# Performance work log

Hardware: AMD Instinct MI355X
Metric: run time of the kernel (lower is better)

The kernel has to match this reference:

```python
import jax, jax.numpy as jnp
import numpy as np

ALPHA = 0.2          # leaky_relu negative slope
NEG_INF = -9e15      # mask fill value (matches torch source)


def setup_inputs() -> dict:
    key = jax.random.key(0)
    k_h, k_mask, k_W, k_a = jax.random.split(key, 4)
    B, N, F_in, F_out = 4, 65536, 128, 128
    h = jax.random.normal(k_h, (B, N, F_in), dtype=jnp.float32)
    # op_mask > 0 means "mask out this neighbor" (prev/self/next)
    op_mask = jax.random.randint(k_mask, (B, N, 3), 0, 2, dtype=jnp.int32)
    # xavier_uniform-style init for params
    lim_W = 1.414 * np.sqrt(6.0 / (F_in + F_out))
    W = jax.random.uniform(k_W, (F_in, F_out), dtype=jnp.float32, minval=-lim_W, maxval=lim_W)
    lim_a = 1.414 * np.sqrt(6.0 / (2 * F_out + 1))
    a = jax.random.uniform(k_a, (2 * F_out, 1), dtype=jnp.float32, minval=-lim_a, maxval=lim_a)
    return {"h": h, "op_mask": op_mask, "W": W, "a": a}


def reference(h, op_mask, W, a):
    F_out = W.shape[1]
    Wh = jnp.matmul(h, W)                                   # [B, N, F]
    # windowed neighbors: prev (roll +1), self, next (roll -1)
    Wh_concat = jnp.stack(
        [jnp.roll(Wh, 1, axis=1), Wh, jnp.roll(Wh, -1, axis=1)], axis=-2
    )                                                       # [B, N, 3, F]
    Wh1 = jnp.matmul(Wh, a[:F_out])                         # [B, N, 1]
    Wh2 = jnp.matmul(Wh, a[F_out:])                         # [B, N, 1]
    Wh2_concat = jnp.stack(
        [jnp.roll(Wh2, 1, axis=1), Wh2, jnp.roll(Wh2, -1, axis=1)], axis=-1
    )                                                       # [B, N, 1, 3]
    e = jax.nn.leaky_relu(Wh1[..., None] + Wh2_concat, ALPHA)  # [B, N, 1, 3]
    e = jnp.where(op_mask[:, :, None, :] > 0, jnp.float32(NEG_INF), e)
    attention = jax.nn.softmax(e, axis=-1)                  # [B, N, 1, 3]
    # dropout_prob = 0.0 (eval-equivalent), so dropout is identity
    h_new = jnp.matmul(attention, Wh_concat).squeeze(-2)    # [B, N, F]
    return h_new
```

## Files before the change

### kernel.cpp

```cpp
#include <hip/hip_runtime.h>
#include <hip/hip_bf16.h>

typedef __attribute__((ext_vector_type(8))) short short8;
typedef __attribute__((ext_vector_type(4))) float f32x4;

#define ALPHA 0.2f
#define NEG_INF -9e15f
#define OUT_ROWS 126

__device__ __forceinline__ unsigned short f2bf(float x) {
    union { float f; unsigned int u; } v; v.f = x;
    unsigned int r = v.u + 0x7FFFu + ((v.u >> 16) & 1u);
    return (unsigned short)(r >> 16);
}

__global__ __launch_bounds__(256, 2)
void gat_fused(const float* __restrict__ h, const int* __restrict__ opm,
               const float* __restrict__ W, const float* __restrict__ a,
               float* __restrict__ out, int N) {
    __shared__ __align__(16) char smem[65536];
    __shared__ float a_s[256];
    __shared__ float wh1_s[128];
    __shared__ float wh2_s[128];
    __shared__ float att_s[128][4];

    const int t = threadIdx.x;
    const int b = blockIdx.y;
    const int row_start = blockIdx.x * OUT_ROWS;
    const int out_rows = min(OUT_ROWS, N - row_start);
    const float* hB = h + (size_t)b * N * 128;
    float* outB = out + (size_t)b * N * 128;

    a_s[t] = a[t];

    #pragma unroll
    for (int i = 0; i < 16; ++i) {
        int idx4 = t + i * 256;
        int k = idx4 >> 5;
        int n4 = (idx4 & 31) << 2;
        float4 w4 = *(const float4*)(W + (k << 7) + n4);
        unsigned short bf[4] = { f2bf(w4.x), f2bf(w4.y), f2bf(w4.z), f2bf(w4.w) };
        #pragma unroll
        for (int j = 0; j < 4; ++j) {
            int jj = j ^ (t & 3);
            int n = n4 + jj;
            *(unsigned short*)(smem + 32768 + n * 256 + ((k * 2) ^ ((n & 7) << 4))) = bf[jj];
        }
    }
    #pragma unroll
    for (int i = 0; i < 16; ++i) {
        int idx4 = t + i * 256;
        int r = idx4 >> 5;
        int c = (idx4 & 31) << 2;
        int g = row_start - 1 + r;
        if (g < 0) g += N;
        if (g >= N) g -= N;
        float4 h4 = *(const float4*)(hB + (size_t)g * 128 + c);
        ushort4 p = make_ushort4(f2bf(h4.x), f2bf(h4.y), f2bf(h4.z), f2bf(h4.w));
        *(ushort4*)(smem + r * 256 + ((c * 2) ^ ((r & 7) << 4))) = p;
    }
    __syncthreads();

    const int lane = t & 63;
    const int wave = t >> 6;
    const int wr = (wave >> 1) << 6;
    const int wc = (wave & 1) << 6;
    const int l15 = lane & 15;
    const int lg = (lane >> 4) & 3;

    f32x4 acc[4][4];
    #pragma unroll
    for (int mi = 0; mi < 4; ++mi)
        #pragma unroll
        for (int ni = 0; ni < 4; ++ni)
            acc[mi][ni] = (f32x4){0.f, 0.f, 0.f, 0.f};

    #pragma unroll
    for (int kk = 0; kk < 4; ++kk) {
        int kbyte = (kk << 6) + (lg << 4);
        short8 af[4], bfr[4];
        #pragma unroll
        for (int mi = 0; mi < 4; ++mi) {
            int m = wr + (mi << 4) + l15;
            af[mi] = *(const short8*)(smem + m * 256 + (kbyte ^ ((m & 7) << 4)));
        }
        #pragma unroll
        for (int ni = 0; ni < 4; ++ni) {
            int n = wc + (ni << 4) + l15;
            bfr[ni] = *(const short8*)(smem + 32768 + n * 256 + (kbyte ^ ((n & 7) << 4)));
        }
        #pragma unroll
        for (int mi = 0; mi < 4; ++mi)
            #pragma unroll
            for (int ni = 0; ni < 4; ++ni)
                acc[mi][ni] = __builtin_amdgcn_mfma_f32_16x16x32_bf16(
                    af[mi], bfr[ni], acc[mi][ni], 0, 0, 0);
    }
    __syncthreads();

    #pragma unroll
    for (int mi = 0; mi < 4; ++mi) {
        #pragma unroll
        for (int ni = 0; ni < 4; ++ni) {
            int col = wc + (ni << 4) + l15;
            #pragma unroll
            for (int j = 0; j < 4; ++j) {
                int row = wr + (mi << 4) + (lg << 2) + j;
                *(float*)(smem + row * 512 + ((col * 4) ^ ((row & 7) << 4))) = acc[mi][ni][j];
            }
        }
    }
    __syncthreads();

    {
        int r = t >> 1;
        int cb = (t & 1) << 6;
        float s1 = 0.f, s2 = 0.f;
        #pragma unroll
        for (int i = 0; i < 16; ++i) {
            int c = cb + (i << 2);
            f32x4 w4 = *(const f32x4*)(smem + r * 512 + ((c * 4) ^ ((r & 7) << 4)));
            s1 += w4[0] * a_s[c] + w4[1] * a_s[c + 1] + w4[2] * a_s[c + 2] + w4[3] * a_s[c + 3];
            s2 += w4[0] * a_s[128 + c] + w4[1] * a_s[129 + c] + w4[2] * a_s[130 + c] + w4[3] * a_s[131 + c];
        }
        s1 += __shfl_xor(s1, 1);
        s2 += __shfl_xor(s2, 1);
        if ((t & 1) == 0) { wh1_s[r] = s1; wh2_s[r] = s2; }
    }
    __syncthreads();

    if (t < 128) {
        int r = t;
        if (r >= 1 && r <= out_rows) {
            int g = row_start + r - 1;
            const int* mr = opm + ((size_t)b * N + g) * 3;
            float w1 = wh1_s[r];
            float e0 = w1 + wh2_s[r - 1];
            float e1 = w1 + wh2_s[r];
            float e2 = w1 + wh2_s[r + 1];
            e0 = e0 > 0.f ? e0 : ALPHA * e0;
            e1 = e1 > 0.f ? e1 : ALPHA * e1;
            e2 = e2 > 0.f ? e2 : ALPHA * e2;
            if (mr[0] > 0) e0 = NEG_INF;
            if (mr[1] > 0) e1 = NEG_INF;
            if (mr[2] > 0) e2 = NEG_INF;
            float m = fmaxf(e0, fmaxf(e1, e2));
            float x0 = expf(e0 - m), x1 = expf(e1 - m), x2 = expf(e2 - m);
            float inv = 1.f / (x0 + x1 + x2);
            att_s[r][0] = x0 * inv;
            att_s[r][1] = x1 * inv;
            att_s[r][2] = x2 * inv;
        }
    }
    __syncthreads();

    for (int it = 0; it < 16; ++it) {
        int r = 1 + (wave << 1) + ((lane >> 5) & 1) + (it << 3);
        if (r > out_rows) continue;
        int c = (lane & 31) << 2;
        float a0 = att_s[r][0], a1 = att_s[r][1], a2 = att_s[r][2];
        f32x4 wm = *(const f32x4*)(smem + (r - 1) * 512 + ((c * 4) ^ (((r - 1) & 7) << 4)));
        f32x4 w0 = *(const f32x4*)(smem + r * 512 + ((c * 4) ^ ((r & 7) << 4)));
        f32x4 wp = *(const f32x4*)(smem + (r + 1) * 512 + ((c * 4) ^ (((r + 1) & 7) << 4)));
        f32x4 res;
        #pragma unroll
        for (int j = 0; j < 4; ++j)
            res[j] = a0 * wm[j] + a1 * w0[j] + a2 * wp[j];
        int g = row_start + r - 1;
        *(f32x4*)(outB + (size_t)g * 128 + c) = res;
    }
}

extern "C" void kernel_launch(void* const* d_in, const int* in_sizes, int n_in,
                              void* d_out, int out_size, void* d_ws, size_t ws_size,
                              hipStream_t stream) {
    const float* h   = (const float*)d_in[0];
    const int*   opm = (const int*)d_in[1];
    const float* W   = (const float*)d_in[2];
    const float* a   = (const float*)d_in[3];
    float* out = (float*)d_out;
    const int N = 65536;
    const int B = 4;
    dim3 grid((N + OUT_ROWS - 1) / OUT_ROWS, B);
    gat_fused<<<grid, 256, 0, stream>>>(h, opm, W, a, out, N);
}
```

Baseline: 65.04 us.

## Prepack W and W·a in prep kernel, async-load h to LDS, fold attention logits into MFMA

```diff
diff --git a/kernel.cpp b/kernel.cpp
--- a/kernel.cpp
+++ b/kernel.cpp
@@ -7,167 +7,215 @@
 #define ALPHA 0.2f
 #define NEG_INF -9e15f
 #define OUT_ROWS 126
-
-__device__ __forceinline__ unsigned short f2bf(float x) {
-    union { float f; unsigned int u; } v; v.f = x;
-    unsigned int r = v.u + 0x7FFFu + ((v.u >> 16) & 1u);
-    return (unsigned short)(r >> 16);
+#define NTILES 521
+#define NB 4
+#define NN 65536
+
+typedef __attribute__((address_space(3))) void as3_void;
+typedef const __attribute__((address_space(1))) void as1_void;
+
+__device__ __forceinline__ short fb(float x) {
+    __hip_bfloat16 b = __float2bfloat16(x);
+    return __builtin_bit_cast(short, b);
+}
+
+__global__ __launch_bounds__(256) void prep_w(const float* __restrict__ W,
+                                              const float* __restrict__ a,
+                                              unsigned short* __restrict__ ws) {
+    const int t = threadIdx.x;
+    if (blockIdx.x < 8) {
+        int q = blockIdx.x * 256 + t;
+        int lane = q & 63, fi = q >> 6;
+        int ni = fi & 3, kk = (fi >> 2) & 3, wcg = fi >> 4;
+        int n = wcg * 64 + ni * 16 + (lane & 15);
+        int k0 = kk * 32 + ((lane >> 4) & 3) * 8;
+        short8 o;
+        #pragma unroll
+        for (int j = 0; j < 8; ++j) o[j] = fb(W[(k0 + j) * 128 + n]);
+        *(short8*)(ws + (size_t)q * 8) = o;
+    } else {
+        __shared__ float wa[2][128];
+        {
+            int k = t >> 1, sel = t & 1;
+            const f32x4* wr4 = (const f32x4*)(W + k * 128);
+            const f32x4* av4 = (const f32x4*)(a + sel * 128);
+            float s = 0.f;
+            #pragma unroll
+            for (int c4 = 0; c4 < 32; ++c4) {
+                f32x4 wv = wr4[c4], av = av4[c4];
+                s += wv[0]*av[0] + wv[1]*av[1] + wv[2]*av[2] + wv[3]*av[3];
+            }
+            wa[sel][k] = s;
+        }
+        __syncthreads();
+        {
+            int lane = t & 63, kk = t >> 6;
+            int l15 = lane & 15, lg = (lane >> 4) & 3;
+            int k0 = kk * 32 + lg * 8;
+            short8 o;
+            #pragma unroll
+            for (int j = 0; j < 8; ++j) {
+                float v = (l15 < 2) ? wa[l15][k0 + j] : 0.f;
+                o[j] = fb(v);
+            }
+            *(short8*)(ws + 16384 + (size_t)t * 8) = o;
+        }
+    }
 }
 
 __global__ __launch_bounds__(256, 2)
 void gat_fused(const float* __restrict__ h, const int* __restrict__ opm,
-               const float* __restrict__ W, const float* __restrict__ a,
-               float* __restrict__ out, int N) {
+               const unsigned short* __restrict__ ws, float* __restrict__ out) {
     __shared__ __align__(16) char smem[65536];
-    __shared__ float a_s[256];
     __shared__ float wh1_s[128];
     __shared__ float wh2_s[128];
     __shared__ float att_s[128][4];
 
     const int t = threadIdx.x;
-    const int b = blockIdx.y;
-    const int row_start = blockIdx.x * OUT_ROWS;
-    const int out_rows = min(OUT_ROWS, N - row_start);
-    const float* hB = h + (size_t)b * N * 128;
-    float* outB = out + (size_t)b * N * 128;
-
-    a_s[t] = a[t];
-
-    #pragma unroll
-    for (int i = 0; i < 16; ++i) {
-        int idx4 = t + i * 256;
-        int k = idx4 >> 5;
-        int n4 = (idx4 & 31) << 2;
-        float4 w4 = *(const float4*)(W + (k << 7) + n4);
-        unsigned short bf[4] = { f2bf(w4.x), f2bf(w4.y), f2bf(w4.z), f2bf(w4.w) };
-        #pragma unroll
-        for (int j = 0; j < 4; ++j) {
-            int jj = j ^ (t & 3);
-            int n = n4 + jj;
-            *(unsigned short*)(smem + 32768 + n * 256 + ((k * 2) ^ ((n & 7) << 4))) = bf[jj];
-        }
-    }
-    #pragma unroll
-    for (int i = 0; i < 16; ++i) {
-        int idx4 = t + i * 256;
-        int r = idx4 >> 5;
-        int c = (idx4 & 31) << 2;
-        int g = row_start - 1 + r;
-        if (g < 0) g += N;
-        if (g >= N) g -= N;
-        float4 h4 = *(const float4*)(hB + (size_t)g * 128 + c);
-        ushort4 p = make_ushort4(f2bf(h4.x), f2bf(h4.y), f2bf(h4.z), f2bf(h4.w));
-        *(ushort4*)(smem + r * 256 + ((c * 2) ^ ((r & 7) << 4))) = p;
-    }
-    __syncthreads();
+    int orig = blockIdx.x;
+    int xcd = orig & 7, idx = orig >> 3;
+    int wgid = (xcd < 4 ? xcd * 261 : 1044 + (xcd - 4) * 260) + idx;
+    const int b = wgid / NTILES;
+    const int tile = wgid - b * NTILES;
+    const int row_start = tile * OUT_ROWS;
+    const int out_rows = min(OUT_ROWS, NN - row_start);
+    const float* hB = h + (size_t)b * NN * 128;
+    float* outB = out + (size_t)b * NN * 128;
 
     const int lane = t & 63;
     const int wave = t >> 6;
-    const int wr = (wave >> 1) << 6;
-    const int wc = (wave & 1) << 6;
+
+    int m0 = 0, m1 = 0, m2 = 0;
+    if (t >= 1 && t <= out_rows) {
+        const int* mr = opm + ((size_t)b * NN + row_start + t - 1) * 3;
+        m0 = mr[0]; m1 = mr[1]; m2 = mr[2];
+    }
+
+    {
+        const char* hC = (const char*)hB;
+        #pragma unroll
+        for (int i = 0; i < 16; ++i) {
+            int rpair = (wave << 4) + i;
+            int r = (rpair << 1) + (lane >> 5);
+            int g = row_start - 1 + r;
+            if (g < 0) g += NN;
+            if (g >= NN) g -= NN;
+            const char* src = hC + (size_t)g * 512 +
+                              (((lane & 31) << 4) ^ ((r & 7) << 4));
+            char* dst = smem + (rpair << 10);
+            __builtin_amdgcn_global_load_lds((as1_void*)src, (as3_void*)dst, 16, 0, 0);
+        }
+    }
+    __syncthreads();
+
     const int l15 = lane & 15;
     const int lg = (lane >> 4) & 3;
+    const int wr = (wave >> 1) << 6;
+    const int wcg = wave & 1;
+    const int wc = wcg << 6;
 
     f32x4 acc[4][4];
-    #pragma unroll
-    for (int mi = 0; mi < 4; ++mi)
+    f32x4 acc2[4];
+    #pragma unroll
+    for (int mi = 0; mi < 4; ++mi) {
+        acc2[mi] = (f32x4){0.f, 0.f, 0.f, 0.f};
         #pragma unroll
         for (int ni = 0; ni < 4; ++ni)
             acc[mi][ni] = (f32x4){0.f, 0.f, 0.f, 0.f};
-
+    }
+
+    const short8* wsv  = (const short8*)ws;
+    const short8* wsv2 = (const short8*)(ws + 16384);
     #pragma unroll
     for (int kk = 0; kk < 4; ++kk) {
-        int kbyte = (kk << 6) + (lg << 4);
-        short8 af[4], bfr[4];
+        short8 bfr[4], bfr2;
+        #pragma unroll
+        for (int ni = 0; ni < 4; ++ni)
+            bfr[ni] = wsv[((((wcg << 2) + kk) << 2) + ni) * 64 + lane];
+        bfr2 = wsv2[(kk << 6) + lane];
+        int kb = (kk << 7) + (lg << 5);
+        short8 af[4];
         #pragma unroll
         for (int mi = 0; mi < 4; ++mi) {
             int m = wr + (mi << 4) + l15;
-            af[mi] = *(const short8*)(smem + m * 256 + (kbyte ^ ((m & 7) << 4)));
-        }
-        #pragma unroll
-        for (int ni = 0; ni < 4; ++ni) {
-            int n = wc + (ni << 4) + l15;
-            bfr[ni] = *(const short8*)(smem + 32768 + n * 256 + (kbyte ^ ((n & 7) << 4)));
-        }
-        #pragma unroll
-        for (int mi = 0; mi < 4; ++mi)
+            int sw = (m & 7) << 4;
+            const char* base = smem + m * 512;
+            f32x4 lo = *(const f32x4*)(base + (kb ^ sw));
+            f32x4 hi = *(const f32x4*)(base + ((kb + 16) ^ sw));
+            short8 v;
+            v[0] = fb(lo[0]); v[1] = fb(lo[1]); v[2] = fb(lo[2]); v[3] = fb(lo[3]);
+            v[4] = fb(hi[0]); v[5] = fb(hi[1]); v[6] = fb(hi[2]); v[7] = fb(hi[3]);
+            af[mi] = v;
+        }
+        #pragma unroll
+        for (int mi = 0; mi < 4; ++mi) {
             #pragma unroll
             for (int ni = 0; ni < 4; ++ni)
                 acc[mi][ni] = __builtin_amdgcn_mfma_f32_16x16x32_bf16(
                     af[mi], bfr[ni], acc[mi][ni], 0, 0, 0);
-    }
-    __syncthreads();
-
-    #pragma unroll
-    for (int mi = 0; mi < 4; ++mi) {
+            acc2[mi] = __builtin_amdgcn_mfma_f32_16x16x32_bf16(
+                af[mi], bfr2, acc2[mi], 0, 0, 0);
+        }
+    }
+    __syncthreads();
+
+    #pragma unroll
+    for (int mi = 0; mi < 4; ++mi)
         #pragma unroll
         for (int ni = 0; ni < 4; ++ni) {
             int col = wc + (ni << 4) + l15;
             #pragma unroll
             for (int j = 0; j < 4; ++j) {
                 int row = wr + (mi << 4) + (lg << 2) + j;
-                *(float*)(smem + row * 512 + ((col * 4) ^ ((row & 7) << 4))) = acc[mi][ni][j];
+                *(float*)(smem + row * 512 + ((col << 2) ^ ((row & 7) << 4))) =
+                    acc[mi][ni][j];
             }
         }
-    }
-    __syncthreads();
-
-    {
-        int r = t >> 1;
-        int cb = (t & 1) << 6;
-        float s1 = 0.f, s2 = 0.f;
-        #pragma unroll
-        for (int i = 0; i < 16; ++i) {
-            int c = cb + (i << 2);
-            f32x4 w4 = *(const f32x4*)(smem + r * 512 + ((c * 4) ^ ((r & 7) << 4)));
-            s1 += w4[0] * a_s[c] + w4[1] * a_s[c + 1] + w4[2] * a_s[c + 2] + w4[3] * a_s[c + 3];
-            s2 += w4[0] * a_s[128 + c] + w4[1] * a_s[129 + c] + w4[2] * a_s[130 + c] + w4[3] * a_s[131 + c];
-        }
-        s1 += __shfl_xor(s1, 1);
-        s2 += __shfl_xor(s2, 1);
-        if ((t & 1) == 0) { wh1_s[r] = s1; wh2_s[r] = s2; }
-    }
-    __syncthreads();
-
-    if (t < 128) {
-        int r = t;
-        if (r >= 1 && r <= out_rows) {
-            int g = row_start + r - 1;
-            const int* mr = opm + ((size_t)b * N + g) * 3;
-            float w1 = wh1_s[r];
-            float e0 = w1 + wh2_s[r - 1];
-            float e1 = w1 + wh2_s[r];
-            float e2 = w1 + wh2_s[r + 1];
-            e0 = e0 > 0.f ? e0 : ALPHA * e0;
-            e1 = e1 > 0.f ? e1 : ALPHA * e1;
-            e2 = e2 > 0.f ? e2 : ALPHA * e2;
-            if (mr[0] > 0) e0 = NEG_INF;
-            if (mr[1] > 0) e1 = NEG_INF;
-            if (mr[2] > 0) e2 = NEG_INF;
-            float m = fmaxf(e0, fmaxf(e1, e2));
-            float x0 = expf(e0 - m), x1 = expf(e1 - m), x2 = expf(e2 - m);
-            float inv = 1.f / (x0 + x1 + x2);
-            att_s[r][0] = x0 * inv;
-            att_s[r][1] = x1 * inv;
-            att_s[r][2] = x2 * inv;
-        }
-    }
-    __syncthreads();
-
+    if (l15 < 2) {
+        float* dv = (l15 == 0) ? wh1_s : wh2_s;
+        #pragma unroll
+        for (int mi = 0; mi < 4; ++mi)
+            #pragma unroll
+            for (int j = 0; j < 4; ++j)
+                dv[wr + (mi << 4) + (lg << 2) + j] = acc2[mi][j];
+    }
+    __syncthreads();
+
+    if (t >= 1 && t <= out_rows) {
+        float w1 = wh1_s[t];
+        float e0 = w1 + wh2_s[t - 1];
+        float e1 = w1 + wh2_s[t];
+        float e2 = w1 + wh2_s[t + 1];
+        e0 = e0 > 0.f ? e0 : ALPHA * e0;
+        e1 = e1 > 0.f ? e1 : ALPHA * e1;
+        e2 = e2 > 0.f ? e2 : ALPHA * e2;
+        if (m0 > 0) e0 = NEG_INF;
+        if (m1 > 0) e1 = NEG_INF;
+        if (m2 > 0) e2 = NEG_INF;
+        float m = fmaxf(e0, fmaxf(e1, e2));
+        float x0 = __expf(e0 - m), x1 = __expf(e1 - m), x2 = __expf(e2 - m);
+        float inv = 1.f / (x0 + x1 + x2);
+        att_s[t][0] = x0 * inv;
+        att_s[t][1] = x1 * inv;
+        att_s[t][2] = x2 * inv;
+    }
+    __syncthreads();
+
+    #pragma unroll
     for (int it = 0; it < 16; ++it) {
-        int r = 1 + (wave << 1) + ((lane >> 5) & 1) + (it << 3);
-        if (r > out_rows) continue;
-        int c = (lane & 31) << 2;
-        float a0 = att_s[r][0], a1 = att_s[r][1], a2 = att_s[r][2];
-        f32x4 wm = *(const f32x4*)(smem + (r - 1) * 512 + ((c * 4) ^ (((r - 1) & 7) << 4)));
-        f32x4 w0 = *(const f32x4*)(smem + r * 512 + ((c * 4) ^ ((r & 7) << 4)));
-        f32x4 wp = *(const f32x4*)(smem + (r + 1) * 512 + ((c * 4) ^ (((r + 1) & 7) << 4)));
+        int rr = 1 + (t >> 5) + (it << 3);
+        if (rr > out_rows) continue;
+        int cb = (t & 31) << 4;
+        float a0 = att_s[rr][0], a1 = att_s[rr][1], a2 = att_s[rr][2];
+        f32x4 wm = *(const f32x4*)(smem + (rr - 1) * 512 + (cb ^ (((rr - 1) & 7) << 4)));
+        f32x4 w0 = *(const f32x4*)(smem + rr * 512 + (cb ^ ((rr & 7) << 4)));
+        f32x4 wp = *(const f32x4*)(smem + (rr + 1) * 512 + (cb ^ (((rr + 1) & 7) << 4)));
         f32x4 res;
         #pragma unroll
         for (int j = 0; j < 4; ++j)
             res[j] = a0 * wm[j] + a1 * w0[j] + a2 * wp[j];
-        int g = row_start + r - 1;
-        *(f32x4*)(outB + (size_t)g * 128 + c) = res;
+        float* op = outB + (size_t)(row_start + rr - 1) * 128 + ((t & 31) << 2);
+        __builtin_nontemporal_store(res, (f32x4*)op);
     }
 }
 
@@ -179,8 +227,7 @@
     const float* W   = (const float*)d_in[2];
     const float* a   = (const float*)d_in[3];
     float* out = (float*)d_out;
-    const int N = 65536;
-    const int B = 4;
-    dim3 grid((N + OUT_ROWS - 1) / OUT_ROWS, B);
-    gat_fused<<<grid, 256, 0, stream>>>(h, opm, W, a, out, N);
-}
+    unsigned short* ws = (unsigned short*)d_ws;
+    prep_w<<<9, 256, 0, stream>>>(W, a, ws);
+    gat_fused<<<NTILES * NB, 256, 0, stream>>>(h, opm, ws, out);
+}
```

New measurement: 64.62 us. About the same (-0.7%).
